# Kernel tuning notes

Hardware: AMD Instinct MI355X
Metric: run time of the kernel (lower is better)

The kernel has to match this reference:

```python
import jax, jax.numpy as jnp
import numpy as np

N, D, H1, K = 4096, 128, 256, 128


def setup_inputs() -> dict:
    key = jax.random.key(0)
    ks = jax.random.split(key, 8)
    A = jax.random.uniform(ks[3], (D, D), dtype=jnp.float32)
    A = A * (1.0 - jnp.eye(D, dtype=jnp.float32))  # DAG prob mask, no self-loops
    return {
        "x": jax.random.normal(ks[0], (N, D), dtype=jnp.float32),
        "weight": jax.random.normal(ks[1], (D, D), dtype=jnp.float32) * 0.1,
        "bias": jax.random.normal(ks[2], (1, D), dtype=jnp.float32) * 0.1,
        "A": A,
        "W1": jax.random.normal(ks[4], (D, H1), dtype=jnp.float32) * 0.1,
        "b1": jax.random.normal(ks[5], (H1,), dtype=jnp.float32) * 0.1,
        "W2": jax.random.normal(ks[6], (H1, K), dtype=jnp.float32) * 0.1,
        "b2": jax.random.normal(ks[7], (K,), dtype=jnp.float32) * 0.1,
    }


def reference(x, weight, bias, A, W1, b1, W2, b2):
    # to_adj (eval path): masked weights
    W = weight * A                                   # [D, D]
    y = x @ W + bias                                 # [N, D]
    # __expand__ builds diag(y[n]) [N,D,D]; since e[n,i,:] = y[n,i]*I[i,:],
    # the first Linear collapses to a per-row scaling of W1 (same math, fused):
    # e @ W1 -> y[n,i] * W1[i,:]
    h1 = jax.nn.relu(y[:, :, None] * W1[None, :, :] + b1)   # [N, D, H1]
    f = (h1 @ W2 + b2).sum(axis=2)                   # [N, D] (sum over output dim)
    # h_func, method='gnn'
    I = jnp.eye(D, dtype=x.dtype)
    A2 = jnp.square(W)
    M = I + A2 / D
    E = jnp.linalg.matrix_power(M, D - 1)
    h_val = (E.T * M).sum() - D
    # l1_reg (same prob mask in eval)
    reg = jnp.abs(W).sum()
    return (f, h_val, reg)
```

## Files before the change

### kernel.cpp

```cpp
#include <hip/hip_runtime.h>

#define NN 4096
#define DD 128
#define HH1 256

#define WS_S    0
#define WS_S2   16384
#define WS_S3   32768
#define WS_S4   49152
#define WS_W    65536
#define WS_W2S  81920
#define WS_PAIR 82176
#define WS_B2S  82688
#define WS_TACC 82696
#define WS_DONE 82708
#define WS_REGP 82712
#define WS_XT   82944
#define WS_YT   607232
#define WS_REQ_FLOATS 1131520
#define WS_REQ_BYTES  (WS_REQ_FLOATS * 4UL)

#define O_S    0
#define O_S2   16384
#define O_S3   32768
#define O_S4   49152
#define O_W2S  65536
#define O_B2S  65792
#define O_TACC 65808
#define O_DONE 65824
#define O_REGP 65840

__device__ __forceinline__ float waveReduce(float v) {
#pragma unroll
  for (int off = 32; off > 0; off >>= 1) v += __shfl_down(v, off, 64);
  return v;
}


__global__ __launch_bounds__(256) void kA2(
    const float* __restrict__ weight, const float* __restrict__ Amat,
    const float* __restrict__ W2, const float* __restrict__ b2,
    const float* __restrict__ b1v, const float* __restrict__ x,
    float* __restrict__ ws) {
  const int b = blockIdx.x, tid = threadIdx.x;
  __shared__ float s_lds[DD * DD];
  __shared__ float xs[128 * 133];
  if (b < 64) {
    const float4* w4 = (const float4*)weight;
    const float4* a4 = (const float4*)Amat;
    float4* s4 = (float4*)s_lds;
    const float inv = 1.0f / 128.0f;
    for (int e = tid; e < DD * DD / 4; e += 256) {
      float4 wv = w4[e], av = a4[e], o;
      float t;
      t = wv.x * av.x; o.x = t * t * inv;
      t = wv.y * av.y; o.y = t * t * inv;
      t = wv.z * av.z; o.z = t * t * inv;
      t = wv.w * av.w; o.w = t * t * inv;
      s4[e] = o;
    }
    __syncthreads();
    const int i = (b << 1) + (tid >> 7), j = tid & 127;
    const float* row = &s_lds[i * DD];
    float acc = 0.f;
#pragma unroll 8
    for (int k = 0; k < DD; ++k) acc = fmaf(row[k], s_lds[k * DD + j], acc);
    ws[WS_S2 + i * DD + j] = acc;
  } else if (b < 72) {
    const int base = (b - 64) * 2048;
    const float inv = 1.0f / 128.0f;
    for (int e = tid; e < 2048; e += 256) {
      const int idx = base + e;
      const float w = weight[idx] * Amat[idx];
      ws[WS_W + idx] = w;
      ws[WS_S + idx] = w * w * inv;
    }
  } else if (b == 72) {
    const float4* r = (const float4*)(W2 + tid * 128);
    float4 s4 = make_float4(0.f, 0.f, 0.f, 0.f);
#pragma unroll 8
    for (int k = 0; k < 32; ++k) {
      const float4 v = r[k];
      s4.x += v.x; s4.y += v.y; s4.z += v.z; s4.w += v.w;
    }
    const float w2sv = (s4.x + s4.y) + (s4.z + s4.w);
    ws[WS_W2S + tid] = w2sv;
    ((float2*)(ws + WS_PAIR))[tid] = make_float2(b1v[tid], w2sv);
  } else if (b == 73) {
    __shared__ float red[4];
    float v = (tid < 128) ? b2[tid] : 0.f;
    v = waveReduce(v);
    if ((tid & 63) == 0) red[tid >> 6] = v;
    __syncthreads();
    if (tid == 0) ws[WS_B2S] = (red[0] + red[1]) + (red[2] + red[3]);
    if (tid >= 64 && tid < 74) ws[WS_TACC + (tid - 64)] = 0.f;
    if (tid == 96) *(unsigned int*)(ws + WS_DONE) = 0u;
  } else if (b < 82) {
    const int bb = b - 74;
    const int base = bb * 2048;
    float s = 0.f;
    for (int e = tid; e < 2048; e += 256) {
      const int idx = base + e;
      s += fabsf(weight[idx] * Amat[idx]);
    }
    s = waveReduce(s);
    __shared__ float red2[4];
    if ((tid & 63) == 0) red2[tid >> 6] = s;
    __syncthreads();
    if (tid == 0) ws[WS_REGP + bb] = (red2[0] + red2[1]) + (red2[2] + red2[3]);
  } else {
    const int n0 = (b - 82) * 128;
    const float4* x4 = (const float4*)x;
    for (int e = tid; e < 4096; e += 256) {
      const int r = e >> 5, c = e & 31;
      const float4 v = x4[(n0 + r) * 32 + c];
      float* p = &xs[r * 133 + (c << 2)];
      p[0] = v.x; p[1] = v.y; p[2] = v.z; p[3] = v.w;
    }
    __syncthreads();
    float* xT = ws + WS_XT;
    const int c = tid & 31, ks = tid >> 5;
#pragma unroll 4
    for (int m = 0; m < 16; ++m) {
      const int k = ks + (m << 3);
      float4 o;
      o.x = xs[((c << 2) + 0) * 133 + k];
      o.y = xs[((c << 2) + 1) * 133 + k];
      o.z = xs[((c << 2) + 2) * 133 + k];
      o.w = xs[((c << 2) + 3) * 133 + k];
      *(float4*)&xT[k * NN + n0 + (c << 2)] = o;
    }
  }
}

__global__ __launch_bounds__(256) void kB2(const float* __restrict__ bias,
                                           float* __restrict__ ws) {
  const int tid = threadIdx.x;
  if (blockIdx.x < 128) {
    const int sb = blockIdx.x;
    const bool isS4 = sb >= 64;
    const int mb = isS4 ? sb - 64 : sb;
    const float* __restrict__ L = ws + WS_S2;
    const float* __restrict__ R = ws + (isS4 ? WS_S2 : WS_S);
    float* __restrict__ O = ws + (isS4 ? WS_S4 : WS_S3);
    const int i = (mb << 1) + (tid >> 7), j = tid & 127;
    float acc = 0.f;
#pragma unroll 8
    for (int k = 0; k < DD; ++k) acc = fmaf(L[i * DD + k], R[k * DD + j], acc);
    O[i * DD + j] = acc;
    return;
  }
  const int kb = blockIdx.x - 128;
  const int n0 = (kb & 15) << 8, i0 = (kb >> 4) << 3;
  const int n = n0 + tid;
  const float* __restrict__ xT = ws + WS_XT;
  const float* __restrict__ Wm = ws + WS_W;
  float* __restrict__ yT = ws + WS_YT;
  float acc[8];
#pragma unroll
  for (int q = 0; q < 8; ++q) acc[q] = 0.f;
#pragma unroll 8
  for (int k = 0; k < DD; ++k) {
    const float xv = xT[k * NN + n];
    const float* Wk = Wm + k * DD + i0;
#pragma unroll
    for (int q = 0; q < 8; ++q) acc[q] = fmaf(Wk[q], xv, acc[q]);
  }
#pragma unroll
  for (int q = 0; q < 8; ++q) yT[(i0 + q) * NN + n] = acc[q] + bias[i0 + q];
}

__global__ __launch_bounds__(256) void kC2(const float* __restrict__ W1,
                                           float* __restrict__ ws,
                                           float* __restrict__ out) {
  const int tid = threadIdx.x;
  if (blockIdx.x < 512) {
    __shared__ float ts[256 * 5];
    const int fb = blockIdx.x;
    const int n0 = (fb >> 5) << 8, i0 = (fb & 31) << 2;
    const int w = tid >> 6, l = tid & 63;
    const int iu = __builtin_amdgcn_readfirstlane(i0 + w);
    const float* __restrict__ yT = ws + WS_YT;
    float t[4];
#pragma unroll
    for (int q = 0; q < 4; ++q) t[q] = yT[iu * NN + n0 + (q << 6) + l];
    const float sb2 = ws[WS_B2S];
    float acc[4];
#pragma unroll
    for (int q = 0; q < 4; ++q) acc[q] = sb2;
    const float* __restrict__ W1row = W1 + iu * HH1;
    const float2* __restrict__ pr = (const float2*)(ws + WS_PAIR);
#pragma unroll 8
    for (int j = 0; j < HH1; ++j) {
      const float sw1 = W1row[j];
      const float2 p = pr[j];
      const float vb = p.x;
#pragma unroll
      for (int q = 0; q < 4; ++q) {
        const float h = fmaxf(fmaf(t[q], sw1, vb), 0.f);
        acc[q] = fmaf(h, p.y, acc[q]);
      }
    }
#pragma unroll
    for (int q = 0; q < 4; ++q) ts[((q << 6) + l) * 5 + w] = acc[q];
    __syncthreads();
    const int m = tid;
    float4 o;
    o.x = ts[m * 5 + 0]; o.y = ts[m * 5 + 1];
    o.z = ts[m * 5 + 2]; o.w = ts[m * 5 + 3];
    *(float4*)&out[(n0 + m) * DD + i0] = o;
    return;
  }
  const int tb = blockIdx.x - 512;
  const int i = (tb << 1) + (tid >> 7), j = tid & 127;
  const float* S1 = ws + WS_S;
  const float* S2 = ws + WS_S2;
  const float* S3 = ws + WS_S3;
  const float* S4 = ws + WS_S4;
  const float a1 = S1[i * DD + j], a2 = S2[i * DD + j], a3 = S3[i * DD + j];
  const float b1t = S1[j * DD + i], b2t = S2[j * DD + i],
              b3t = S3[j * DD + i], b4t = S4[j * DD + i];
  float e7 = 0.f;
#pragma unroll 8
  for (int k = 0; k < DD; ++k) e7 = fmaf(S3[i * DD + k], S4[k * DD + j], e7);
  float c[10];
  c[0] = a1 * b1t; c[1] = a2 * b1t; c[2] = a2 * b2t; c[3] = a3 * b2t;
  c[4] = a3 * b3t; c[5] = a3 * b4t; c[6] = e7 * b1t; c[7] = e7 * b2t;
  c[8] = e7 * b3t; c[9] = e7 * b4t;
  __shared__ float red[4][10];
#pragma unroll
  for (int m = 0; m < 10; ++m) {
    const float v = waveReduce(c[m]);
    if ((tid & 63) == 0) red[tid >> 6][m] = v;
  }
  __syncthreads();
  if (tid == 0) {
    float* tacc = ws + WS_TACC;
    for (int m = 0; m < 10; ++m)
      atomicAdd(&tacc[m], (red[0][m] + red[1][m]) + (red[2][m] + red[3][m]));
    __threadfence();
    unsigned int* done = (unsigned int*)(ws + WS_DONE);
    const unsigned int old = atomicAdd(done, 1u);
    if (old == 63u) {
      __threadfence();
      double h = 0.0, C = 8128.0;
      for (int kk = 2; kk <= 11; ++kk) {
        const float tv = atomicAdd(&tacc[kk - 2], 0.0f);
        h += C * (double)tv;
        C = C * (double)(128 - kk) / (double)(kk + 1);
      }
      float reg = 0.f;
      for (int m = 0; m < 8; ++m) reg += ws[WS_REGP + m];
      out[NN * DD] = (float)h;
      out[NN * DD + 1] = reg;
    }
  }
}

__global__ __launch_bounds__(256) void kA_old(
    const float* __restrict__ weight, const float* __restrict__ Amat,
    const float* __restrict__ W2, const float* __restrict__ b2,
    float* __restrict__ ws) {
  const int b = blockIdx.x, tid = threadIdx.x;
  if (b < 64) {
    __shared__ float s_lds[DD * DD];
    const float4* w4 = (const float4*)weight;
    const float4* a4 = (const float4*)Amat;
    float4* s4 = (float4*)s_lds;
    const float inv = 1.0f / 128.0f;
    for (int e = tid; e < DD * DD / 4; e += 256) {
      float4 wv = w4[e], av = a4[e], o;
      float t;
      t = wv.x * av.x; o.x = t * t * inv;
      t = wv.y * av.y; o.y = t * t * inv;
      t = wv.z * av.z; o.z = t * t * inv;
      t = wv.w * av.w; o.w = t * t * inv;
      s4[e] = o;
    }
    __syncthreads();
    const int i = (b << 1) + (tid >> 7), j = tid & 127;
    const float* row = &s_lds[i * DD];
    float acc = 0.f;
#pragma unroll 8
    for (int k = 0; k < DD; ++k) acc = fmaf(row[k], s_lds[k * DD + j], acc);
    ws[O_S2 + i * DD + j] = acc;
  } else if (b < 72) {
    const int base = (b - 64) * 2048;
    const float inv = 1.0f / 128.0f;
    for (int e = tid; e < 2048; e += 256) {
      const int idx = base + e;
      const float w = weight[idx] * Amat[idx];
      ws[O_S + idx] = w * w * inv;
    }
  } else if (b == 72) {
    const float4* r = (const float4*)(W2 + tid * 128);
    float4 s4 = make_float4(0.f, 0.f, 0.f, 0.f);
#pragma unroll 8
    for (int k = 0; k < 32; ++k) {
      const float4 v = r[k];
      s4.x += v.x; s4.y += v.y; s4.z += v.z; s4.w += v.w;
    }
    ws[O_W2S + tid] = (s4.x + s4.y) + (s4.z + s4.w);
  } else if (b == 73) {
    __shared__ float red[4];
    float v = (tid < 128) ? b2[tid] : 0.f;
    v = waveReduce(v);
    if ((tid & 63) == 0) red[tid >> 6] = v;
    __syncthreads();
    if (tid == 0) ws[O_B2S] = (red[0] + red[1]) + (red[2] + red[3]);
    if (tid >= 64 && tid < 74) ws[O_TACC + (tid - 64)] = 0.f;
    if (tid == 96) *(unsigned int*)(ws + O_DONE) = 0u;
  } else {
    const int bb = b - 74;
    const int base = bb * 2048;
    float s = 0.f;
    for (int e = tid; e < 2048; e += 256) {
      const int idx = base + e;
      s += fabsf(weight[idx] * Amat[idx]);
    }
    s = waveReduce(s);
    __shared__ float red[4];
    if ((tid & 63) == 0) red[tid >> 6] = s;
    __syncthreads();
    if (tid == 0) ws[O_REGP + bb] = (red[0] + red[1]) + (red[2] + red[3]);
  }
}

__global__ __launch_bounds__(256) void kB_old(
    const float* __restrict__ x, const float* __restrict__ weight,
    const float* __restrict__ Amat, const float* __restrict__ bias,
    const float* __restrict__ W1, const float* __restrict__ b1v,
    float* __restrict__ ws, float* __restrict__ out) {
  const int tid = threadIdx.x;
  if (blockIdx.x < 128) {
    const int sb = blockIdx.x;
    const bool isS4 = sb >= 64;
    const int mb = isS4 ? sb - 64 : sb;
    const float* __restrict__ L = ws + O_S2;
    const float* __restrict__ R = ws + (isS4 ? O_S2 : O_S);
    float* __restrict__ O = ws + (isS4 ? O_S4 : O_S3);
    const int i = (mb << 1) + (tid >> 7), j = tid & 127;
    float acc = 0.f;
#pragma unroll 8
    for (int k = 0; k < DD; ++k) acc = fmaf(L[i * DD + k], R[k * DD + j], acc);
    O[i * DD + j] = acc;
    return;
  }
  __shared__ float xs[64 * 132];
  __shared__ float4 fq[4 * 256];
  __shared__ float wcol[4 * 128];
  __shared__ float ts[64 * 5];
  const int fb = blockIdx.x - 128;
  const int i0 = (fb & 31) << 2, n0 = (fb >> 5) << 6;
  const float4* x4 = (const float4*)x;
  for (int e = tid; e < 64 * 32; e += 256) {
    const int r = e >> 5, c = e & 31;
    *(float4*)&xs[r * 132 + (c << 2)] = x4[(n0 + r) * 32 + c];
  }
  for (int e = tid; e < 512; e += 256) {
    const int w = e >> 7, k = e & 127;
    const int gi = k * DD + i0 + w;
    wcol[(w << 7) + k] = weight[gi] * Amat[gi];
  }
  const float* w2s = ws + O_W2S;
  for (int e = tid; e < 1024; e += 256) {
    const int w = e >> 8, j = e & 255;
    fq[(w << 8) + j] = make_float4(W1[(i0 + w) * HH1 + j], b1v[j], w2s[j], 0.f);
  }
  __syncthreads();
  const int w = tid >> 6, l = tid & 63;
  float t = bias[i0 + w];
  const float4* xr = (const float4*)&xs[l * 132];
  const float4* wc = (const float4*)&wcol[w << 7];
#pragma unroll
  for (int k = 0; k < 32; ++k) {
    const float4 xv = xr[k], wv = wc[k];
    t = fmaf(xv.x, wv.x, t);
    t = fmaf(xv.y, wv.y, t);
    t = fmaf(xv.z, wv.z, t);
    t = fmaf(xv.w, wv.w, t);
  }
  float acc = ws[O_B2S];
  const float4* fp = &fq[w << 8];
#pragma unroll 8
  for (int j = 0; j < HH1; ++j) {
    const float4 c = fp[j];
    acc = fmaf(fmaxf(fmaf(t, c.x, c.y), 0.f), c.z, acc);
  }
  ts[l * 5 + w] = acc;
  __syncthreads();
  if (tid < 64) {
    const float4 o = make_float4(ts[tid * 5 + 0], ts[tid * 5 + 1],
                                 ts[tid * 5 + 2], ts[tid * 5 + 3]);
    *(float4*)&out[(n0 + tid) * DD + i0] = o;
  }
}

__global__ __launch_bounds__(256) void kC_old(float* __restrict__ ws,
                                              float* __restrict__ out) {
  const int tid = threadIdx.x;
  const int i = (blockIdx.x << 1) + (tid >> 7), j = tid & 127;
  const float* S1 = ws + O_S;
  const float* S2 = ws + O_S2;
  const float* S3 = ws + O_S3;
  const float* S4 = ws + O_S4;
  const float a1 = S1[i * DD + j], a2 = S2[i * DD + j], a3 = S3[i * DD + j];
  const float b1t = S1[j * DD + i], b2t = S2[j * DD + i],
              b3t = S3[j * DD + i], b4t = S4[j * DD + i];
  float e7 = 0.f;
#pragma unroll 8
  for (int k = 0; k < DD; ++k) e7 = fmaf(S3[i * DD + k], S4[k * DD + j], e7);
  float c[10];
  c[0] = a1 * b1t; c[1] = a2 * b1t; c[2] = a2 * b2t; c[3] = a3 * b2t;
  c[4] = a3 * b3t; c[5] = a3 * b4t; c[6] = e7 * b1t; c[7] = e7 * b2t;
  c[8] = e7 * b3t; c[9] = e7 * b4t;
  __shared__ float red[4][10];
#pragma unroll
  for (int m = 0; m < 10; ++m) {
    const float v = waveReduce(c[m]);
    if ((tid & 63) == 0) red[tid >> 6][m] = v;
  }
  __syncthreads();
  if (tid == 0) {
    float* tacc = ws + O_TACC;
    for (int m = 0; m < 10; ++m)
      atomicAdd(&tacc[m], (red[0][m] + red[1][m]) + (red[2][m] + red[3][m]));
    __threadfence();
    unsigned int* done = (unsigned int*)(ws + O_DONE);
    const unsigned int old = atomicAdd(done, 1u);
    if (old == 63u) {
      __threadfence();
      double h = 0.0, C = 8128.0;
      for (int kk = 2; kk <= 11; ++kk) {
        const float tv = atomicAdd(&tacc[kk - 2], 0.0f);
        h += C * (double)tv;
        C = C * (double)(128 - kk) / (double)(kk + 1);
      }
      float reg = 0.f;
      for (int m = 0; m < 8; ++m) reg += ws[O_REGP + m];
      out[NN * DD] = (float)h;
      out[NN * DD + 1] = reg;
    }
  }
}

extern "C" void kernel_launch(void* const* d_in, const int* in_sizes, int n_in,
                              void* d_out, int out_size, void* d_ws,
                              size_t ws_size, hipStream_t stream) {
  const float* x      = (const float*)d_in[0];
  const float* weight = (const float*)d_in[1];
  const float* bias   = (const float*)d_in[2];
  const float* Amat   = (const float*)d_in[3];
  const float* W1     = (const float*)d_in[4];
  const float* b1v    = (const float*)d_in[5];
  const float* W2     = (const float*)d_in[6];
  const float* b2     = (const float*)d_in[7];
  float* out = (float*)d_out;
  float* ws  = (float*)d_ws;

  if (ws_size >= WS_REQ_BYTES) {
    kA2<<<114, 256, 0, stream>>>(weight, Amat, W2, b2, b1v, x, ws);
    kB2<<<384, 256, 0, stream>>>(bias, ws);
    kC2<<<576, 256, 0, stream>>>(W1, ws, out);
  } else {
    kA_old<<<82, 256, 0, stream>>>(weight, Amat, W2, b2, ws);
    kB_old<<<128 + 2048, 256, 0, stream>>>(x, weight, Amat, bias, W1, b1v, ws,
                                           out);
    kC_old<<<64, 256, 0, stream>>>(ws, out);
  }
}
```

Baseline: 109.6 us.

## Fuse y=xW GEMM into the MLP kernel and drop the yT workspace round trip

The x@W+bias product is now computed inside the same blocks that evaluate the per-element MLP. Each block stages x^T chunks in shared memory and computes its 8 rows of y for 256 samples, so y never goes through global memory. The S3/S4 matrix products move into this kernel with 512-thread blocks, leaving a smaller final kernel for the trace reduction. The cost is lower parallelism in the y computation (each wave handles one output column), a larger shared-memory footprint per block, and extra barriers.

Result: slower. 116.3 us (+6.1%).

```diff
diff --git a/kernel.cpp b/kernel.cpp
--- a/kernel.cpp
+++ b/kernel.cpp
@@ -16,8 +16,7 @@
 #define WS_DONE 82708
 #define WS_REGP 82712
 #define WS_XT   82944
-#define WS_YT   607232
-#define WS_REQ_FLOATS 1131520
+#define WS_REQ_FLOATS 607232
 #define WS_REQ_BYTES  (WS_REQ_FLOATS * 4UL)
 
 #define O_S    0
@@ -133,85 +132,98 @@
   }
 }
 
-__global__ __launch_bounds__(256) void kB2(const float* __restrict__ bias,
-                                           float* __restrict__ ws) {
+__global__ __launch_bounds__(512) void kB3(const float* __restrict__ bias,
+                                           const float* __restrict__ W1,
+                                           float* __restrict__ ws,
+                                           float* __restrict__ out) {
   const int tid = threadIdx.x;
-  if (blockIdx.x < 128) {
+  if (blockIdx.x < 64) {
     const int sb = blockIdx.x;
-    const bool isS4 = sb >= 64;
-    const int mb = isS4 ? sb - 64 : sb;
+    const bool isS4 = sb >= 32;
+    const int mb = isS4 ? sb - 32 : sb;
     const float* __restrict__ L = ws + WS_S2;
     const float* __restrict__ R = ws + (isS4 ? WS_S2 : WS_S);
     float* __restrict__ O = ws + (isS4 ? WS_S4 : WS_S3);
-    const int i = (mb << 1) + (tid >> 7), j = tid & 127;
+    const int i = (mb << 2) + (tid >> 7), j = tid & 127;
     float acc = 0.f;
 #pragma unroll 8
     for (int k = 0; k < DD; ++k) acc = fmaf(L[i * DD + k], R[k * DD + j], acc);
     O[i * DD + j] = acc;
     return;
   }
-  const int kb = blockIdx.x - 128;
-  const int n0 = (kb & 15) << 8, i0 = (kb >> 4) << 3;
-  const int n = n0 + tid;
+  const int fb = blockIdx.x - 64;
+  const int n0 = (fb & 15) << 8;
+  const int i0 = (fb >> 4) << 3;
+  const int w = tid >> 6, l = tid & 63;
+  __shared__ float xs[32][256];
+  __shared__ float ts[256][9];
   const float* __restrict__ xT = ws + WS_XT;
   const float* __restrict__ Wm = ws + WS_W;
-  float* __restrict__ yT = ws + WS_YT;
-  float acc[8];
-#pragma unroll
-  for (int q = 0; q < 8; ++q) acc[q] = 0.f;
-#pragma unroll 8
-  for (int k = 0; k < DD; ++k) {
-    const float xv = xT[k * NN + n];
-    const float* Wk = Wm + k * DD + i0;
-#pragma unroll
-    for (int q = 0; q < 8; ++q) acc[q] = fmaf(Wk[q], xv, acc[q]);
-  }
-#pragma unroll
-  for (int q = 0; q < 8; ++q) yT[(i0 + q) * NN + n] = acc[q] + bias[i0 + q];
-}
-
-__global__ __launch_bounds__(256) void kC2(const float* __restrict__ W1,
-                                           float* __restrict__ ws,
+  const int iu = __builtin_amdgcn_readfirstlane(i0 + w);
+
+  float t[4] = {0.f, 0.f, 0.f, 0.f};
+  for (int kc = 0; kc < 4; ++kc) {
+    __syncthreads();
+    {
+      const float4* src = (const float4*)(xT + (kc * 32) * NN + n0);
+      float4* dst4 = (float4*)&xs[0][0];
+#pragma unroll
+      for (int m = 0; m < 4; ++m) {
+        const int e = tid + (m << 9);
+        const int kk = e >> 6, c = e & 63;
+        dst4[(kk << 6) + c] = src[kk * (NN / 4) + c];
+      }
+    }
+    __syncthreads();
+#pragma unroll
+    for (int kk = 0; kk < 32; ++kk) {
+      const float wv = Wm[(kc * 32 + kk) * DD + iu];
+      const float4 xv = *(const float4*)&xs[kk][l << 2];
+      t[0] = fmaf(xv.x, wv, t[0]);
+      t[1] = fmaf(xv.y, wv, t[1]);
+      t[2] = fmaf(xv.z, wv, t[2]);
+      t[3] = fmaf(xv.w, wv, t[3]);
+    }
+  }
+  const float bv = bias[iu];
+#pragma unroll
+  for (int q = 0; q < 4; ++q) t[q] += bv;
+
+  const float sb2 = ws[WS_B2S];
+  float acc[4];
+#pragma unroll
+  for (int q = 0; q < 4; ++q) acc[q] = sb2;
+  const float* __restrict__ W1row = W1 + iu * HH1;
+  const float2* __restrict__ pr = (const float2*)(ws + WS_PAIR);
+#pragma unroll 8
+  for (int j = 0; j < HH1; ++j) {
+    const float sw1 = W1row[j];
+    const float2 p = pr[j];
+    const float vb = p.x;
+#pragma unroll
+    for (int q = 0; q < 4; ++q) {
+      const float h = fmaxf(fmaf(t[q], sw1, vb), 0.f);
+      acc[q] = fmaf(h, p.y, acc[q]);
+    }
+  }
+#pragma unroll
+  for (int q = 0; q < 4; ++q) ts[(l << 2) + q][w] = acc[q];
+  __syncthreads();
+  {
+    const int m = tid >> 1, half = tid & 1;
+    float4 o;
+    o.x = ts[m][(half << 2) + 0];
+    o.y = ts[m][(half << 2) + 1];
+    o.z = ts[m][(half << 2) + 2];
+    o.w = ts[m][(half << 2) + 3];
+    *(float4*)&out[(n0 + m) * DD + i0 + (half << 2)] = o;
+  }
+}
+
+__global__ __launch_bounds__(256) void kC3(float* __restrict__ ws,
                                            float* __restrict__ out) {
   const int tid = threadIdx.x;
-  if (blockIdx.x < 512) {
-    __shared__ float ts[256 * 5];
-    const int fb = blockIdx.x;
-    const int n0 = (fb >> 5) << 8, i0 = (fb & 31) << 2;
-    const int w = tid >> 6, l = tid & 63;
-    const int iu = __builtin_amdgcn_readfirstlane(i0 + w);
-    const float* __restrict__ yT = ws + WS_YT;
-    float t[4];
-#pragma unroll
-    for (int q = 0; q < 4; ++q) t[q] = yT[iu * NN + n0 + (q << 6) + l];
-    const float sb2 = ws[WS_B2S];
-    float acc[4];
-#pragma unroll
-    for (int q = 0; q < 4; ++q) acc[q] = sb2;
-    const float* __restrict__ W1row = W1 + iu * HH1;
-    const float2* __restrict__ pr = (const float2*)(ws + WS_PAIR);
-#pragma unroll 8
-    for (int j = 0; j < HH1; ++j) {
-      const float sw1 = W1row[j];
-      const float2 p = pr[j];
-      const float vb = p.x;
-#pragma unroll
-      for (int q = 0; q < 4; ++q) {
-        const float h = fmaxf(fmaf(t[q], sw1, vb), 0.f);
-        acc[q] = fmaf(h, p.y, acc[q]);
-      }
-    }
-#pragma unroll
-    for (int q = 0; q < 4; ++q) ts[((q << 6) + l) * 5 + w] = acc[q];
-    __syncthreads();
-    const int m = tid;
-    float4 o;
-    o.x = ts[m * 5 + 0]; o.y = ts[m * 5 + 1];
-    o.z = ts[m * 5 + 2]; o.w = ts[m * 5 + 3];
-    *(float4*)&out[(n0 + m) * DD + i0] = o;
-    return;
-  }
-  const int tb = blockIdx.x - 512;
+  const int tb = blockIdx.x;
   const int i = (tb << 1) + (tid >> 7), j = tid & 127;
   const float* S1 = ws + WS_S;
   const float* S2 = ws + WS_S2;
@@ -460,8 +472,8 @@
 
   if (ws_size >= WS_REQ_BYTES) {
     kA2<<<114, 256, 0, stream>>>(weight, Amat, W2, b2, b1v, x, ws);
-    kB2<<<384, 256, 0, stream>>>(bias, ws);
-    kC2<<<576, 256, 0, stream>>>(W1, ws, out);
+    kB3<<<320, 512, 0, stream>>>(bias, W1, ws, out);
+    kC3<<<64, 256, 0, stream>>>(ws, out);
   } else {
     kA_old<<<82, 256, 0, stream>>>(weight, Amat, W2, b2, ws);
     kB_old<<<128 + 2048, 256, 0, stream>>>(x, weight, Amat, bias, W1, b1v, ws,
```

## Fuse x@W projection into f-compute kernel, drop yT intermediate buffer

Applied to the files above, without the earlier changes.

Moves the y = xW + bias computation out of the middle kernel and into the per-(row-block, column) blocks of the final kernel, so the 2 MB yT intermediate is never written or read back. The middle kernel now only computes S3/S4 with 128 blocks. The cost is redundant work: each wave recomputes a 128-length dot product for its 256 rows. This lightens the middle launch but makes the f blocks longer. Output shared-memory indexing is adjusted for the new float4 row mapping.

Measured after the change: 125.8 us. +14.8%, slower.

```diff
diff --git a/kernel.cpp b/kernel.cpp
--- a/kernel.cpp
+++ b/kernel.cpp
@@ -16,8 +16,7 @@
 #define WS_DONE 82708
 #define WS_REGP 82712
 #define WS_XT   82944
-#define WS_YT   607232
-#define WS_REQ_FLOATS 1131520
+#define WS_REQ_FLOATS 607232
 #define WS_REQ_BYTES  (WS_REQ_FLOATS * 4UL)
 
 #define O_S    0
@@ -133,44 +132,23 @@
   }
 }
 
-__global__ __launch_bounds__(256) void kB2(const float* __restrict__ bias,
-                                           float* __restrict__ ws) {
+__global__ __launch_bounds__(256) void kS34(float* __restrict__ ws) {
   const int tid = threadIdx.x;
-  if (blockIdx.x < 128) {
-    const int sb = blockIdx.x;
-    const bool isS4 = sb >= 64;
-    const int mb = isS4 ? sb - 64 : sb;
-    const float* __restrict__ L = ws + WS_S2;
-    const float* __restrict__ R = ws + (isS4 ? WS_S2 : WS_S);
-    float* __restrict__ O = ws + (isS4 ? WS_S4 : WS_S3);
-    const int i = (mb << 1) + (tid >> 7), j = tid & 127;
-    float acc = 0.f;
-#pragma unroll 8
-    for (int k = 0; k < DD; ++k) acc = fmaf(L[i * DD + k], R[k * DD + j], acc);
-    O[i * DD + j] = acc;
-    return;
-  }
-  const int kb = blockIdx.x - 128;
-  const int n0 = (kb & 15) << 8, i0 = (kb >> 4) << 3;
-  const int n = n0 + tid;
-  const float* __restrict__ xT = ws + WS_XT;
-  const float* __restrict__ Wm = ws + WS_W;
-  float* __restrict__ yT = ws + WS_YT;
-  float acc[8];
-#pragma unroll
-  for (int q = 0; q < 8; ++q) acc[q] = 0.f;
-#pragma unroll 8
-  for (int k = 0; k < DD; ++k) {
-    const float xv = xT[k * NN + n];
-    const float* Wk = Wm + k * DD + i0;
-#pragma unroll
-    for (int q = 0; q < 8; ++q) acc[q] = fmaf(Wk[q], xv, acc[q]);
-  }
-#pragma unroll
-  for (int q = 0; q < 8; ++q) yT[(i0 + q) * NN + n] = acc[q] + bias[i0 + q];
-}
-
-__global__ __launch_bounds__(256) void kC2(const float* __restrict__ W1,
+  const int sb = blockIdx.x;
+  const bool isS4 = sb >= 64;
+  const int mb = isS4 ? sb - 64 : sb;
+  const float* __restrict__ L = ws + WS_S2;
+  const float* __restrict__ R = ws + (isS4 ? WS_S2 : WS_S);
+  float* __restrict__ O = ws + (isS4 ? WS_S4 : WS_S3);
+  const int i = (mb << 1) + (tid >> 7), j = tid & 127;
+  float acc = 0.f;
+#pragma unroll 8
+  for (int k = 0; k < DD; ++k) acc = fmaf(L[i * DD + k], R[k * DD + j], acc);
+  O[i * DD + j] = acc;
+}
+
+__global__ __launch_bounds__(256) void kC4(const float* __restrict__ W1,
+                                           const float* __restrict__ bias,
                                            float* __restrict__ ws,
                                            float* __restrict__ out) {
   const int tid = threadIdx.x;
@@ -180,10 +158,23 @@
     const int n0 = (fb >> 5) << 8, i0 = (fb & 31) << 2;
     const int w = tid >> 6, l = tid & 63;
     const int iu = __builtin_amdgcn_readfirstlane(i0 + w);
-    const float* __restrict__ yT = ws + WS_YT;
-    float t[4];
-#pragma unroll
-    for (int q = 0; q < 4; ++q) t[q] = yT[iu * NN + n0 + (q << 6) + l];
+    const float* __restrict__ xT = ws + WS_XT;
+    const float* __restrict__ Wm = ws + WS_W;
+
+    float t[4] = {0.f, 0.f, 0.f, 0.f};
+#pragma unroll 8
+    for (int k = 0; k < DD; ++k) {
+      const float wv = Wm[k * DD + iu];
+      const float4 xv = *(const float4*)&xT[k * NN + n0 + (l << 2)];
+      t[0] = fmaf(xv.x, wv, t[0]);
+      t[1] = fmaf(xv.y, wv, t[1]);
+      t[2] = fmaf(xv.z, wv, t[2]);
+      t[3] = fmaf(xv.w, wv, t[3]);
+    }
+    const float bv = bias[iu];
+#pragma unroll
+    for (int q = 0; q < 4; ++q) t[q] += bv;
+
     const float sb2 = ws[WS_B2S];
     float acc[4];
 #pragma unroll
@@ -202,7 +193,7 @@
       }
     }
 #pragma unroll
-    for (int q = 0; q < 4; ++q) ts[((q << 6) + l) * 5 + w] = acc[q];
+    for (int q = 0; q < 4; ++q) ts[((l << 2) + q) * 5 + w] = acc[q];
     __syncthreads();
     const int m = tid;
     float4 o;
@@ -460,8 +451,8 @@
 
   if (ws_size >= WS_REQ_BYTES) {
     kA2<<<114, 256, 0, stream>>>(weight, Amat, W2, b2, b1v, x, ws);
-    kB2<<<384, 256, 0, stream>>>(bias, ws);
-    kC2<<<576, 256, 0, stream>>>(W1, ws, out);
+    kS34<<<128, 256, 0, stream>>>(ws);
+    kC4<<<576, 256, 0, stream>>>(W1, bias, ws, out);
   } else {
     kA_old<<<82, 256, 0, stream>>>(weight, Amat, W2, b2, ws);
     kB_old<<<128 + 2048, 256, 0, stream>>>(x, weight, Amat, bias, W1, b1v, ws,
```
